# Performance work log

Measured on AMD Instinct MI355X. Metric: run time of the kernel, lower is better.

## Reference

```python
import jax, jax.numpy as jnp
import numpy as np

B, S, D, H = 8, 1024, 768, 16
PD = D // H  # projection dims per head


def setup_inputs() -> dict:
    key = jax.random.key(0)
    ks = jax.random.split(key, 9)
    s = 1.0 / np.sqrt(D)
    return {
        "inputs": jax.random.normal(ks[0], (B, S, D), dtype=jnp.float32),
        "Wq": jax.random.normal(ks[1], (D, D), dtype=jnp.float32) * s,
        "bq": jnp.zeros((D,), dtype=jnp.float32),
        "Wk": jax.random.normal(ks[2], (D, D), dtype=jnp.float32) * s,
        "bk": jnp.zeros((D,), dtype=jnp.float32),
        "Wv": jax.random.normal(ks[3], (D, D), dtype=jnp.float32) * s,
        "bv": jnp.zeros((D,), dtype=jnp.float32),
        "Wo": jax.random.normal(ks[4], (D, D), dtype=jnp.float32) * s,
        "bo": jnp.zeros((D,), dtype=jnp.float32),
    }


def _split_heads(x):
    # [B,S,D] -> [B,H,S,PD]
    return x.reshape(B, S, H, PD).transpose(0, 2, 1, 3)


def reference(inputs, Wq, bq, Wk, bk, Wv, bv, Wo, bo):
    q = _split_heads(inputs @ Wq + bq)
    k = _split_heads(inputs @ Wk + bk)
    v = _split_heads(inputs @ Wv + bv)
    scale = 1.0 / jnp.sqrt(jnp.asarray(PD, dtype=q.dtype))
    scores = jnp.einsum("bhqd,bhkd->bhqk", q, k) * scale
    weights = jax.nn.softmax(scores, axis=-1)
    attn = jnp.einsum("bhqk,bhkd->bhqd", weights, v)
    concat = attn.transpose(0, 2, 1, 3).reshape(B, S, D)
    return concat @ Wo + bo
```

## Files before the change

kernel.cpp:

```cpp
#include <hip/hip_runtime.h>
#include <hip/hip_bf16.h>

#define B_   8
#define S_   1024
#define D_   768
#define H_   16
#define PD_  48
#define PDP  64
#define M_   8192
#define BH_  128

#define QSCALE 0.20823031f

typedef __attribute__((ext_vector_type(8))) short short8;
typedef __attribute__((ext_vector_type(4))) float floatx4;

__device__ __forceinline__ unsigned short f2bf(float f) {
    __hip_bfloat16 h = __float2bfloat16(f);
    return *reinterpret_cast<unsigned short*>(&h);
}

__device__ __forceinline__ void async_copy16(const unsigned short* gptr, unsigned short* lptr) {
    __builtin_amdgcn_global_load_lds(
        (const __attribute__((address_space(1))) unsigned int*)gptr,
        (__attribute__((address_space(3))) unsigned int*)lptr, 16, 0, 0);
}

__global__ __launch_bounds__(256) void convert_x_kernel(
    const float* __restrict__ X, unsigned short* __restrict__ Xb) {
    long i = ((long)blockIdx.x * 256 + threadIdx.x) * 4;
    float4 v = *(const float4*)(X + i);
    ushort4 o;
    o.x = f2bf(v.x); o.y = f2bf(v.y); o.z = f2bf(v.z); o.w = f2bf(v.w);
    *(ushort4*)(Xb + i) = o;
}

__global__ __launch_bounds__(256) void transpose_w_kernel(
    const float* __restrict__ w0, const float* __restrict__ w1,
    const float* __restrict__ w2, const float* __restrict__ w3,
    unsigned short* __restrict__ Wtall) {
    __shared__ float tile[32][33];
    const int tx = threadIdx.x, ty = threadIdx.y;
    const int nt = blockIdx.x * 32, kt = blockIdx.y * 32, z = blockIdx.z;
    const float* W = (z == 0) ? w0 : (z == 1) ? w1 : (z == 2) ? w2 : w3;
    unsigned short* Wt = Wtall + (long)z * D_ * D_;
#pragma unroll
    for (int i = 0; i < 4; i++)
        tile[ty + i * 8][tx] = W[(long)(kt + ty + i * 8) * D_ + nt + tx];
    __syncthreads();
#pragma unroll
    for (int i = 0; i < 4; i++)
        Wt[(long)(nt + ty + i * 8) * D_ + kt + tx] = f2bf(tile[tx][ty + i * 8]);
}

__device__ __forceinline__ void gemm_core(
    const unsigned short* __restrict__ Ag,
    const unsigned short* __restrict__ Btg,
    unsigned short* Asm, unsigned short* Bsm, floatx4 acc[4][4]) {
    const int tid = threadIdx.x;
    const int lane = tid & 63, w = tid >> 6;
    const int wr = (w >> 1) * 64, wc = (w & 1) * 64;
    const int l15 = lane & 15, l4 = lane >> 4;
    const floatx4 zero = {0.f, 0.f, 0.f, 0.f};
#pragma unroll
    for (int mt = 0; mt < 4; mt++)
#pragma unroll
        for (int nt = 0; nt < 4; nt++) acc[mt][nt] = zero;

    for (int kb = 0; kb < D_; kb += 64) {
#pragma unroll
        for (int i = 0; i < 4; i++) {
            int c = tid + i * 256;
            int row = c >> 3, seg = (c & 7) ^ (row & 7);
            long goff = (long)row * D_ + kb + seg * 8;
            async_copy16(&Ag[goff], &Asm[c * 8]);
            async_copy16(&Btg[goff], &Bsm[c * 8]);
        }
        __syncthreads();
#pragma unroll
        for (int kk = 0; kk < 2; kk++) {
            short8 af[4], bf[4];
#pragma unroll
            for (int mt = 0; mt < 4; mt++) {
                int r = wr + mt * 16 + l15;
                af[mt] = *(const short8*)&Asm[r * 64 + (((kk * 4 + l4) ^ (r & 7)) * 8)];
            }
#pragma unroll
            for (int nt = 0; nt < 4; nt++) {
                int c = wc + nt * 16 + l15;
                bf[nt] = *(const short8*)&Bsm[c * 64 + (((kk * 4 + l4) ^ (c & 7)) * 8)];
            }
#pragma unroll
            for (int mt = 0; mt < 4; mt++)
#pragma unroll
                for (int nt = 0; nt < 4; nt++)
                    acc[mt][nt] = __builtin_amdgcn_mfma_f32_16x16x32_bf16(
                        af[mt], bf[nt], acc[mt][nt], 0, 0, 0);
        }
        __syncthreads();
    }
}

__global__ __launch_bounds__(256) void gemm_qkv_kernel(
    const unsigned short* __restrict__ Xb, const unsigned short* __restrict__ Wtall,
    const float* __restrict__ bq, const float* __restrict__ bk,
    const float* __restrict__ bv, unsigned short* __restrict__ QKV) {
    __shared__ __align__(16) unsigned short Asm[128 * 64];
    __shared__ __align__(16) unsigned short Bsm[128 * 64];
    const int z = blockIdx.z;
    const int m0 = blockIdx.y * 128, n0 = blockIdx.x * 128;
    const float* bias = (z == 0) ? bq : (z == 1) ? bk : bv;
    const float vscale = (z == 0) ? QSCALE : 1.0f;
    floatx4 acc[4][4];
    gemm_core(Xb + (long)m0 * D_, Wtall + (long)z * D_ * D_ + (long)n0 * D_, Asm, Bsm, acc);

    unsigned short* out = QKV + (long)z * BH_ * S_ * PDP;
    const int tid = threadIdx.x, lane = tid & 63, w = tid >> 6;
    const int wr = (w >> 1) * 64, wc = (w & 1) * 64;
    const int l15 = lane & 15, l4 = lane >> 4;
#pragma unroll
    for (int nt = 0; nt < 4; nt++) {
        int n = n0 + wc + nt * 16 + l15;
        int h = n / PD_, pd = n % PD_;
        float bb = bias[n];
#pragma unroll
        for (int mt = 0; mt < 4; mt++) {
#pragma unroll
            for (int r = 0; r < 4; r++) {
                int m = m0 + wr + mt * 16 + l4 * 4 + r;
                int b = m >> 10, s = m & 1023;
                out[((long)(b * H_ + h) * S_ + s) * PDP + pd] = f2bf((acc[mt][nt][r] + bb) * vscale);
            }
        }
    }
}

__global__ __launch_bounds__(256) void transpose_v_kernel(
    const unsigned short* __restrict__ V, unsigned short* __restrict__ Vt) {
    __shared__ __align__(16) unsigned short T[64 * 64];
    const int tid = threadIdx.x;
    const int st = blockIdx.x * 64, bh = blockIdx.y;
    const unsigned short* src = V + (long)bh * S_ * PDP;
    unsigned short* dst = Vt + (long)bh * PDP * S_;
#pragma unroll
    for (int i = 0; i < 2; i++) {
        int c = tid + i * 256;
        int row = c >> 3, seg = (c & 7) ^ (row & 7);
        async_copy16(&src[(long)(st + row) * PDP + seg * 8], &T[c * 8]);
    }
    __syncthreads();
    const int d = tid >> 2;
    unsigned short tmp[16];
#pragma unroll
    for (int j = 0; j < 16; j++) {
        int sl = (tid & 3) * 16 + j;
        unsigned short v = T[sl * 64 + ((d >> 3) ^ (sl & 7)) * 8 + (d & 7)];
        tmp[j] = (d < PD_) ? v : ((d == PD_) ? (unsigned short)0x3F80 : (unsigned short)0);
    }
    *(uint4*)&dst[(long)d * S_ + st + (tid & 3) * 16] = *(uint4*)&tmp[0];
    *(uint4*)&dst[(long)d * S_ + st + (tid & 3) * 16 + 8] = *(uint4*)&tmp[8];
}

__global__ __launch_bounds__(256) void gemm_out_kernel(
    const unsigned short* __restrict__ Ctx, const unsigned short* __restrict__ Wot,
    const float* __restrict__ bo, float* __restrict__ Out) {
    __shared__ __align__(16) unsigned short Asm[128 * 64];
    __shared__ __align__(16) unsigned short Bsm[128 * 64];
    const int m0 = blockIdx.y * 128, n0 = blockIdx.x * 128;
    floatx4 acc[4][4];
    gemm_core(Ctx + (long)m0 * D_, Wot + (long)n0 * D_, Asm, Bsm, acc);

    const int tid = threadIdx.x, lane = tid & 63, w = tid >> 6;
    const int wr = (w >> 1) * 64, wc = (w & 1) * 64;
    const int l15 = lane & 15, l4 = lane >> 4;
#pragma unroll
    for (int nt = 0; nt < 4; nt++) {
        int n = n0 + wc + nt * 16 + l15;
        float bb = bo[n];
#pragma unroll
        for (int mt = 0; mt < 4; mt++) {
#pragma unroll
            for (int r = 0; r < 4; r++) {
                int m = m0 + wr + mt * 16 + l4 * 4 + r;
                Out[(long)m * D_ + n] = acc[mt][nt][r] + bb;
            }
        }
    }
}

__global__ __launch_bounds__(256, 4) void attn_kernel(
    const unsigned short* __restrict__ Qg, const unsigned short* __restrict__ Kg,
    const unsigned short* __restrict__ Vtg, unsigned short* __restrict__ Ctx) {
    __shared__ __align__(16) unsigned short Ks[64 * 64];
    __shared__ __align__(16) unsigned short Vs[64 * 64];
    __shared__ __align__(16) unsigned short Ps[4][16 * 64];
    const int tid = threadIdx.x, lane = tid & 63, w = tid >> 6;
    const int l15 = lane & 15, l4 = lane >> 4;
    const int qt = blockIdx.x, bh = blockIdx.y;
    const long qkbase = (long)bh * S_ * PDP;
    const long vbase  = (long)bh * PDP * S_;

    short8 bq[2][2];
#pragma unroll
    for (int g = 0; g < 2; g++) {
        int qrow = qt * 128 + w * 32 + g * 16 + l15;
        bq[g][0] = *(const short8*)&Qg[qkbase + (long)qrow * PDP + l4 * 8];
        bq[g][1] = *(const short8*)&Qg[qkbase + (long)qrow * PDP + 32 + l4 * 8];
    }

    const floatx4 zero = {0.f, 0.f, 0.f, 0.f};
    floatx4 accO[2][4];
#pragma unroll
    for (int g = 0; g < 2; g++)
#pragma unroll
        for (int nt = 0; nt < 4; nt++) accO[g][nt] = zero;

    unsigned short* Pw = &Ps[w][0];

    for (int kt = 0; kt < 16; kt++) {
        __syncthreads();
#pragma unroll
        for (int i = 0; i < 2; i++) {
            int c = tid + i * 256;
            int row = c >> 3, seg = (c & 7) ^ (row & 7);
            async_copy16(&Kg[qkbase + (long)(kt * 64 + row) * PDP + seg * 8], &Ks[c * 8]);
            async_copy16(&Vtg[vbase + (long)row * S_ + kt * 64 + seg * 8], &Vs[c * 8]);
        }
        __syncthreads();

        short8 ak[4][2];
#pragma unroll
        for (int ks = 0; ks < 4; ks++) {
            int kr = ks * 16 + l15;
            ak[ks][0] = *(const short8*)&Ks[kr * 64 + ((l4 ^ (kr & 7)) * 8)];
            ak[ks][1] = *(const short8*)&Ks[kr * 64 + (((4 + l4) ^ (kr & 7)) * 8)];
        }

#pragma unroll
        for (int g = 0; g < 2; g++) {
            floatx4 sc[4];
#pragma unroll
            for (int ks = 0; ks < 4; ks++) {
                floatx4 a = zero;
                a = __builtin_amdgcn_mfma_f32_16x16x32_bf16(ak[ks][0], bq[g][0], a, 0, 0, 0);
                a = __builtin_amdgcn_mfma_f32_16x16x32_bf16(ak[ks][1], bq[g][1], a, 0, 0, 0);
                sc[ks] = a;
            }
#pragma unroll
            for (int ks = 0; ks < 4; ks++) {
                unsigned short p4[4];
#pragma unroll
                for (int r = 0; r < 4; r++) p4[r] = f2bf(__builtin_amdgcn_exp2f(sc[ks][r]));
                int addr = l15 * 64 + (((ks * 2 + (l4 >> 1)) ^ (l15 & 7)) * 8) + (l4 & 1) * 4;
                *(uint2*)&Pw[addr] = *(uint2*)&p4[0];
            }
#pragma unroll
            for (int kk = 0; kk < 2; kk++) {
                short8 ap = *(const short8*)&Pw[l15 * 64 + (((kk * 4 + l4) ^ (l15 & 7)) * 8)];
#pragma unroll
                for (int nt = 0; nt < 4; nt++) {
                    int vr = nt * 16 + l15;
                    short8 bv8 = *(const short8*)&Vs[vr * 64 + (((kk * 4 + l4) ^ (vr & 7)) * 8)];
                    accO[g][nt] = __builtin_amdgcn_mfma_f32_16x16x32_bf16(ap, bv8, accO[g][nt], 0, 0, 0);
                }
            }
        }
    }

    const int b = bh >> 4, h = bh & 15;
#pragma unroll
    for (int g = 0; g < 2; g++) {
#pragma unroll
        for (int r = 0; r < 4; r++) {
            float lsum = __shfl(accO[g][3][r], lane & 48);
            float inv = 1.0f / lsum;
            int q = qt * 128 + w * 32 + g * 16 + l4 * 4 + r;
            long rowoff = (long)(b * S_ + q) * D_ + h * PD_;
#pragma unroll
            for (int nt = 0; nt < 3; nt++)
                Ctx[rowoff + nt * 16 + l15] = f2bf(accO[g][nt][r] * inv);
        }
    }
}

extern "C" void kernel_launch(void* const* d_in, const int* in_sizes, int n_in,
                              void* d_out, int out_size, void* d_ws, size_t ws_size,
                              hipStream_t stream) {
    const float* X  = (const float*)d_in[0];
    const float* Wq = (const float*)d_in[1];
    const float* bq = (const float*)d_in[2];
    const float* Wk = (const float*)d_in[3];
    const float* bk = (const float*)d_in[4];
    const float* Wv = (const float*)d_in[5];
    const float* bv = (const float*)d_in[6];
    const float* Wo = (const float*)d_in[7];
    const float* bo = (const float*)d_in[8];

    unsigned char* ws = (unsigned char*)d_ws;
    const long XB_BYTES  = (long)M_ * D_ * 2;
    const long WT_BYTES  = (long)D_ * D_ * 2;
    const long QKV_BYTES = (long)BH_ * S_ * PDP * 2;

    unsigned short* Xbf   = (unsigned short*)(ws);
    unsigned short* Wtall = (unsigned short*)(ws + XB_BYTES);
    unsigned short* Qws   = (unsigned short*)(ws + XB_BYTES + 4 * WT_BYTES);
    unsigned short* Kws   = Qws + QKV_BYTES / 2;
    unsigned short* Vws   = Kws + QKV_BYTES / 2;
    unsigned short* Vtws  = Vws + QKV_BYTES / 2;
    unsigned short* Ctx   = Vws;

    hipMemsetAsync(Qws, 0, 2 * QKV_BYTES, stream);

    convert_x_kernel<<<(M_ * D_) / (256 * 4), 256, 0, stream>>>(X, Xbf);
    transpose_w_kernel<<<dim3(24, 24, 4), dim3(32, 8), 0, stream>>>(Wq, Wk, Wv, Wo, Wtall);
    gemm_qkv_kernel<<<dim3(6, 64, 3), 256, 0, stream>>>(Xbf, Wtall, bq, bk, bv, Qws);
    transpose_v_kernel<<<dim3(16, 128), 256, 0, stream>>>(Vws, Vtws);
    attn_kernel<<<dim3(8, 128), 256, 0, stream>>>(Qws, Kws, Vtws, Ctx);
    gemm_out_kernel<<<dim3(6, 64), 256, 0, stream>>>(
        Ctx, Wtall + 3 * (WT_BYTES / 2), bo, (float*)d_out);
}
```

Measured before the change: 219.6 us.

## Fuse prep kernels, drop memset, enlarge attention query tile, reorder grids

After: 195.9 us. -10.8%, faster.

```diff
diff --git a/kernel.cpp b/kernel.cpp
--- a/kernel.cpp
+++ b/kernel.cpp
@@ -26,22 +26,26 @@
         (__attribute__((address_space(3))) unsigned int*)lptr, 16, 0, 0);
 }
 
-__global__ __launch_bounds__(256) void convert_x_kernel(
-    const float* __restrict__ X, unsigned short* __restrict__ Xb) {
-    long i = ((long)blockIdx.x * 256 + threadIdx.x) * 4;
-    float4 v = *(const float4*)(X + i);
-    ushort4 o;
-    o.x = f2bf(v.x); o.y = f2bf(v.y); o.z = f2bf(v.z); o.w = f2bf(v.w);
-    *(ushort4*)(Xb + i) = o;
-}
-
-__global__ __launch_bounds__(256) void transpose_w_kernel(
+__global__ __launch_bounds__(256) void prep_kernel(
+    const float* __restrict__ X, unsigned short* __restrict__ Xb,
     const float* __restrict__ w0, const float* __restrict__ w1,
     const float* __restrict__ w2, const float* __restrict__ w3,
     unsigned short* __restrict__ Wtall) {
     __shared__ float tile[32][33];
-    const int tx = threadIdx.x, ty = threadIdx.y;
-    const int nt = blockIdx.x * 32, kt = blockIdx.y * 32, z = blockIdx.z;
+    const int tid = threadIdx.x;
+    const int bx = blockIdx.x;
+    if (bx < 6144) {
+        long i = ((long)bx * 256 + tid) * 4;
+        float4 v = *(const float4*)(X + i);
+        ushort4 o;
+        o.x = f2bf(v.x); o.y = f2bf(v.y); o.z = f2bf(v.z); o.w = f2bf(v.w);
+        *(ushort4*)(Xb + i) = o;
+        return;
+    }
+    const int t = bx - 6144;
+    const int z = t / 576, r = t % 576;
+    const int nt = (r % 24) * 32, kt = (r / 24) * 32;
+    const int tx = tid & 31, ty = tid >> 5;
     const float* W = (z == 0) ? w0 : (z == 1) ? w1 : (z == 2) ? w2 : w3;
     unsigned short* Wt = Wtall + (long)z * D_ * D_;
 #pragma unroll
@@ -108,7 +112,7 @@
     __shared__ __align__(16) unsigned short Asm[128 * 64];
     __shared__ __align__(16) unsigned short Bsm[128 * 64];
     const int z = blockIdx.z;
-    const int m0 = blockIdx.y * 128, n0 = blockIdx.x * 128;
+    const int m0 = blockIdx.x * 128, n0 = blockIdx.y * 128;
     const float* bias = (z == 0) ? bq : (z == 1) ? bk : bv;
     const float vscale = (z == 0) ? QSCALE : 1.0f;
     floatx4 acc[4][4];
@@ -166,7 +170,7 @@
     const float* __restrict__ bo, float* __restrict__ Out) {
     __shared__ __align__(16) unsigned short Asm[128 * 64];
     __shared__ __align__(16) unsigned short Bsm[128 * 64];
-    const int m0 = blockIdx.y * 128, n0 = blockIdx.x * 128;
+    const int m0 = blockIdx.x * 128, n0 = blockIdx.y * 128;
     floatx4 acc[4][4];
     gemm_core(Ctx + (long)m0 * D_, Wot + (long)n0 * D_, Asm, Bsm, acc);
 
@@ -188,30 +192,35 @@
     }
 }
 
-__global__ __launch_bounds__(256, 4) void attn_kernel(
+__global__ __launch_bounds__(256) void attn_kernel(
     const unsigned short* __restrict__ Qg, const unsigned short* __restrict__ Kg,
     const unsigned short* __restrict__ Vtg, unsigned short* __restrict__ Ctx) {
     __shared__ __align__(16) unsigned short Ks[64 * 64];
     __shared__ __align__(16) unsigned short Vs[64 * 64];
-    __shared__ __align__(16) unsigned short Ps[4][16 * 64];
+    __shared__ __align__(16) unsigned short Ps[4][64 * 64];
     const int tid = threadIdx.x, lane = tid & 63, w = tid >> 6;
     const int l15 = lane & 15, l4 = lane >> 4;
-    const int qt = blockIdx.x, bh = blockIdx.y;
+    const int bh = blockIdx.x, qt = blockIdx.y;
     const long qkbase = (long)bh * S_ * PDP;
     const long vbase  = (long)bh * PDP * S_;
 
-    short8 bq[2][2];
-#pragma unroll
-    for (int g = 0; g < 2; g++) {
-        int qrow = qt * 128 + w * 32 + g * 16 + l15;
+    short8 bq[4][2];
+#pragma unroll
+    for (int g = 0; g < 4; g++) {
+        int qrow = qt * 256 + w * 64 + g * 16 + l15;
         bq[g][0] = *(const short8*)&Qg[qkbase + (long)qrow * PDP + l4 * 8];
         bq[g][1] = *(const short8*)&Qg[qkbase + (long)qrow * PDP + 32 + l4 * 8];
     }
+    if (l4 >= 2) {
+        const short8 z8 = {0, 0, 0, 0, 0, 0, 0, 0};
+#pragma unroll
+        for (int g = 0; g < 4; g++) bq[g][1] = z8;
+    }
 
     const floatx4 zero = {0.f, 0.f, 0.f, 0.f};
-    floatx4 accO[2][4];
-#pragma unroll
-    for (int g = 0; g < 2; g++)
+    floatx4 accO[4][4];
+#pragma unroll
+    for (int g = 0; g < 4; g++)
 #pragma unroll
         for (int nt = 0; nt < 4; nt++) accO[g][nt] = zero;
 
@@ -237,7 +246,7 @@
         }
 
 #pragma unroll
-        for (int g = 0; g < 2; g++) {
+        for (int g = 0; g < 4; g++) {
             floatx4 sc[4];
 #pragma unroll
             for (int ks = 0; ks < 4; ks++) {
@@ -246,35 +255,44 @@
                 a = __builtin_amdgcn_mfma_f32_16x16x32_bf16(ak[ks][1], bq[g][1], a, 0, 0, 0);
                 sc[ks] = a;
             }
+            int prow = g * 16 + l15;
 #pragma unroll
             for (int ks = 0; ks < 4; ks++) {
                 unsigned short p4[4];
 #pragma unroll
                 for (int r = 0; r < 4; r++) p4[r] = f2bf(__builtin_amdgcn_exp2f(sc[ks][r]));
-                int addr = l15 * 64 + (((ks * 2 + (l4 >> 1)) ^ (l15 & 7)) * 8) + (l4 & 1) * 4;
+                int addr = prow * 64 + (((ks * 2 + (l4 >> 1)) ^ (prow & 7)) * 8) + (l4 & 1) * 4;
                 *(uint2*)&Pw[addr] = *(uint2*)&p4[0];
             }
-#pragma unroll
-            for (int kk = 0; kk < 2; kk++) {
-                short8 ap = *(const short8*)&Pw[l15 * 64 + (((kk * 4 + l4) ^ (l15 & 7)) * 8)];
-#pragma unroll
-                for (int nt = 0; nt < 4; nt++) {
-                    int vr = nt * 16 + l15;
-                    short8 bv8 = *(const short8*)&Vs[vr * 64 + (((kk * 4 + l4) ^ (vr & 7)) * 8)];
-                    accO[g][nt] = __builtin_amdgcn_mfma_f32_16x16x32_bf16(ap, bv8, accO[g][nt], 0, 0, 0);
-                }
+        }
+
+#pragma unroll
+        for (int kk = 0; kk < 2; kk++) {
+            short8 bv[4];
+#pragma unroll
+            for (int nt = 0; nt < 4; nt++) {
+                int vr = nt * 16 + l15;
+                bv[nt] = *(const short8*)&Vs[vr * 64 + (((kk * 4 + l4) ^ (vr & 7)) * 8)];
+            }
+#pragma unroll
+            for (int g = 0; g < 4; g++) {
+                int prow = g * 16 + l15;
+                short8 ap = *(const short8*)&Pw[prow * 64 + (((kk * 4 + l4) ^ (prow & 7)) * 8)];
+#pragma unroll
+                for (int nt = 0; nt < 4; nt++)
+                    accO[g][nt] = __builtin_amdgcn_mfma_f32_16x16x32_bf16(ap, bv[nt], accO[g][nt], 0, 0, 0);
             }
         }
     }
 
     const int b = bh >> 4, h = bh & 15;
 #pragma unroll
-    for (int g = 0; g < 2; g++) {
+    for (int g = 0; g < 4; g++) {
 #pragma unroll
         for (int r = 0; r < 4; r++) {
             float lsum = __shfl(accO[g][3][r], lane & 48);
             float inv = 1.0f / lsum;
-            int q = qt * 128 + w * 32 + g * 16 + l4 * 4 + r;
+            int q = qt * 256 + w * 64 + g * 16 + l4 * 4 + r;
             long rowoff = (long)(b * S_ + q) * D_ + h * PD_;
 #pragma unroll
             for (int nt = 0; nt < 3; nt++)
@@ -309,13 +327,10 @@
     unsigned short* Vtws  = Vws + QKV_BYTES / 2;
     unsigned short* Ctx   = Vws;
 
-    hipMemsetAsync(Qws, 0, 2 * QKV_BYTES, stream);
-
-    convert_x_kernel<<<(M_ * D_) / (256 * 4), 256, 0, stream>>>(X, Xbf);
-    transpose_w_kernel<<<dim3(24, 24, 4), dim3(32, 8), 0, stream>>>(Wq, Wk, Wv, Wo, Wtall);
-    gemm_qkv_kernel<<<dim3(6, 64, 3), 256, 0, stream>>>(Xbf, Wtall, bq, bk, bv, Qws);
+    prep_kernel<<<8448, 256, 0, stream>>>(X, Xbf, Wq, Wk, Wv, Wo, Wtall);
+    gemm_qkv_kernel<<<dim3(64, 6, 3), 256, 0, stream>>>(Xbf, Wtall, bq, bk, bv, Qws);
     transpose_v_kernel<<<dim3(16, 128), 256, 0, stream>>>(Vws, Vtws);
-    attn_kernel<<<dim3(8, 128), 256, 0, stream>>>(Qws, Kws, Vtws, Ctx);
-    gemm_out_kernel<<<dim3(6, 64), 256, 0, stream>>>(
+    attn_kernel<<<dim3(128, 4), 256, 0, stream>>>(Qws, Kws, Vtws, Ctx);
+    gemm_out_kernel<<<dim3(64, 6), 256, 0, stream>>>(
         Ctx, Wtall + 3 * (WT_BYTES / 2), bo, (float*)d_out);
 }
```
